# Kernel tuning notes

Hardware: AMD Instinct MI355X
Metric: run time of the kernel (lower is better)

Reference implementation:

```python
import jax, jax.numpy as jnp
import numpy as np

N, E, C = 50000, 800000, 100000
D_IN, HID = 128, 128
MLP_IN, MLP_HID = 2 * HID + 1, HID // 2
BN_EPS = 1e-5
NEG_SLOPE = 0.01


def setup_inputs() -> dict:
    key = jax.random.key(0)
    ks = jax.random.split(key, 24)
    inp = {
        "x": jax.random.normal(ks[0], (N, D_IN), jnp.float32),
        "src": jax.random.randint(ks[1], (E,), 0, N, jnp.int32),
        "dst": jax.random.randint(ks[2], (E,), 0, N, jnp.int32),
        "cand_u": jax.random.randint(ks[3], (C,), 0, N, jnp.int32),
        "cand_v": jax.random.randint(ks[4], (C,), 0, N, jnp.int32),
        "cand_feat": jax.random.normal(ks[5], (C, 1), jnp.float32),
    }
    s = 1.0 / np.sqrt(D_IN)
    # SAGEConv layer 0 and 1 (in=out=128 since statedim == pnhid)
    for li, k0 in [(0, 6), (1, 12)]:
        inp[f"w_self{li}"] = jax.random.uniform(ks[k0], (D_IN, HID), jnp.float32, -s, s)
        inp[f"w_neigh{li}"] = jax.random.uniform(ks[k0 + 1], (D_IN, HID), jnp.float32, -s, s)
        inp[f"b{li}"] = jnp.zeros((HID,), jnp.float32)
        inp[f"gamma{li}"] = jnp.ones((HID,), jnp.float32)
        inp[f"beta{li}"] = jnp.zeros((HID,), jnp.float32)
        inp[f"rm{li}"] = jax.random.normal(ks[k0 + 2], (HID,), jnp.float32) * 0.1
        inp[f"rv{li}"] = jax.random.uniform(ks[k0 + 3], (HID,), jnp.float32, 0.5, 1.5)
    # confidence MLP: 257 -> 64 -> 64 -> 1
    sizes = [MLP_IN, MLP_HID, MLP_HID, 1]
    for i in range(3):
        si = 1.0 / np.sqrt(sizes[i])
        inp[f"mw{i}"] = jax.random.uniform(ks[18 + 2 * i], (sizes[i], sizes[i + 1]), jnp.float32, -si, si)
        inp[f"mb{i}"] = jax.random.uniform(ks[19 + 2 * i], (sizes[i + 1],), jnp.float32, -si, si)
    return inp


def _sage_bn_block(x, src, dst, w_self, w_neigh, b, gamma, beta, rm, rv):
    # mean aggregation over incoming edges (gather -> scatter-add -> divide)
    msgs = x[src]  # [E, D]
    agg = jax.ops.segment_sum(msgs, dst, num_segments=N)  # [N, D]
    deg = jax.ops.segment_sum(jnp.ones((src.shape[0],), x.dtype), dst, num_segments=N)
    agg = agg / jnp.maximum(deg, 1.0)[:, None]
    h = x @ w_self + agg @ w_neigh + b
    # BatchNorm1d (eval mode, running stats) then leaky_relu; dropout is identity in eval
    h = gamma * (h - rm) * jax.lax.rsqrt(rv + BN_EPS) + beta
    return jax.nn.leaky_relu(h, NEG_SLOPE)


def reference(x, src, dst, cand_u, cand_v, cand_feat,
              w_self0, w_neigh0, b0, gamma0, beta0, rm0, rv0,
              w_self1, w_neigh1, b1, gamma1, beta1, rm1, rv1,
              mw0, mb0, mw1, mb1, mw2, mb2):
    h = _sage_bn_block(x, src, dst, w_self0, w_neigh0, b0, gamma0, beta0, rm0, rv0)
    h = _sage_bn_block(h, src, dst, w_self1, w_neigh1, b1, gamma1, beta1, rm1, rv1)
    h = jnp.nan_to_num(h, nan=1e-14)
    # candidate embeddings: [C, 2*HID + 1]
    ce = jnp.concatenate([h[cand_u], h[cand_v], cand_feat], axis=-1)
    z = jax.nn.leaky_relu(ce @ mw0 + mb0, NEG_SLOPE)
    z = jax.nn.leaky_relu(z @ mw1 + mb1, NEG_SLOPE)
    y = z @ mw2 + mb2  # [C, 1]
    return y, jax.nn.softmax(y, axis=0)
```

## Files before the change

### kernel.cpp

```cpp
#include <hip/hip_runtime.h>
#include <math.h>

#define N_NODES 50000
#define N_EDGES 800000
#define N_CAND  100000
#define D       128
#define BN_EPS  1e-5f
#define SLOPE   0.01f

#define NB2     196
#define TILE    4096
#define NTILE   196
#define BCAP    4736

typedef __attribute__((ext_vector_type(8))) short bf16x8;
typedef __attribute__((ext_vector_type(4))) float f32x4;

__device__ __forceinline__ float lrelu(float x){ return x >= 0.f ? x : SLOPE * x; }

__device__ __forceinline__ unsigned short f2bf_rn(float f){
  unsigned int u = __float_as_uint(f);
  unsigned int r = u + 0x7FFFu + ((u >> 16) & 1u);
  return (unsigned short)(r >> 16);
}
__device__ __forceinline__ float bf2f(unsigned short h){
  return __uint_as_float(((unsigned int)h) << 16);
}
__device__ __forceinline__ float4 bf4f(ushort4 u){
  return make_float4(__uint_as_float((unsigned)u.x << 16),
                     __uint_as_float((unsigned)u.y << 16),
                     __uint_as_float((unsigned)u.z << 16),
                     __uint_as_float((unsigned)u.w << 16));
}

__device__ __forceinline__ unsigned pk_bf16(float a, float b){
  unsigned r;
  asm("v_cvt_pk_bf16_f32 %0, %1, %2" : "=v"(r) : "v"(a), "v"(b));
  return r;
}
__device__ __forceinline__ void split2(float a, float b, unsigned &h, unsigned &l){
  h = pk_bf16(a, b);
  float ra = a - __uint_as_float(h << 16);
  float rb = b - __uint_as_float(h & 0xffff0000u);
  l = pk_bf16(ra, rb);
}
__device__ __forceinline__ void split8(const float4 &v0, const float4 &v1, uint4 &h, uint4 &l){
  split2(v0.x, v0.y, h.x, l.x);
  split2(v0.z, v0.w, h.y, l.y);
  split2(v1.x, v1.y, h.z, l.z);
  split2(v1.z, v1.w, h.w, l.w);
}

__global__ __launch_bounds__(256) void k_bin(const int* __restrict__ src, const int* __restrict__ dst,
                                             int* __restrict__ gcnt, unsigned* __restrict__ ebin, int E){
  __shared__ unsigned stage[TILE];
  __shared__ int hist[256], lscan[256], lex[256], lcur[256], gbase[256];
  __shared__ int stot;
  int t = threadIdx.x;
  int e0 = blockIdx.x * TILE;

  hist[t] = 0;
  __syncthreads();

  unsigned pk[16]; int bk[16]; bool ok[16];
  #pragma unroll
  for (int j = 0; j < 16; ++j){
    int i = e0 + j * 256 + t;
    ok[j] = (i < E);
    if (ok[j]){
      int d = dst[i];
      pk[j] = ((unsigned)d << 16) | (unsigned)src[i];
      bk[j] = d >> 8;
      atomicAdd(&hist[bk[j]], 1);
    }
  }
  __syncthreads();

  lscan[t] = hist[t];
  __syncthreads();
  for (int off = 1; off < 256; off <<= 1){
    int v = (t >= off) ? lscan[t - off] : 0;
    __syncthreads();
    lscan[t] += v;
    __syncthreads();
  }
  int ex = lscan[t] - hist[t];
  lex[t]  = ex;
  lcur[t] = ex;
  if (t < NB2) gbase[t] = hist[t] ? atomicAdd(&gcnt[t], hist[t]) : 0;
  if (t == 255) stot = lscan[255];
  __syncthreads();

  #pragma unroll
  for (int j = 0; j < 16; ++j){
    if (ok[j]){
      int p = atomicAdd(&lcur[bk[j]], 1);
      stage[p] = pk[j];
    }
  }
  __syncthreads();

  int tot = stot;
  for (int i = t; i < tot; i += 256){
    unsigned e = stage[i];
    int b = (int)(e >> 24);
    ebin[(size_t)b * BCAP + gbase[b] + (i - lex[b])] = e;
  }
}

__global__ __launch_bounds__(256) void k_bscan2(const int* __restrict__ gcnt, int* __restrict__ bbase,
                                                int* __restrict__ rowptr){
  __shared__ int sd[256];
  int t = threadIdx.x;
  int v = (t < NB2) ? gcnt[t] : 0;
  sd[t] = v; __syncthreads();
  for (int off = 1; off < 256; off <<= 1){
    int a = (t >= off) ? sd[t - off] : 0;
    __syncthreads();
    sd[t] += a; __syncthreads();
  }
  if (t < NB2) bbase[t] = sd[t] - v;
  if (t == NB2 - 1) rowptr[N_NODES] = sd[t];
}

__global__ __launch_bounds__(256) void k_bfin(const int* __restrict__ gcnt, const int* __restrict__ bbase,
                                              const unsigned* __restrict__ ebin,
                                              unsigned short* __restrict__ eid16,
                                              int* __restrict__ rowptr, int n){
  __shared__ int hist[256], lb[256], lcur[256];
  int t = threadIdx.x, b = blockIdx.x;
  int cb   = gcnt[b];
  int base = bbase[b];
  const unsigned* eb = &ebin[(size_t)b * BCAP];
  hist[t] = 0;
  __syncthreads();
  for (int idx = t; idx < cb; idx += 256) atomicAdd(&hist[(eb[idx] >> 16) & 255], 1);
  __syncthreads();
  lb[t] = hist[t];
  __syncthreads();
  for (int off = 1; off < 256; off <<= 1){
    int v = (t >= off) ? lb[t - off] : 0;
    __syncthreads();
    lb[t] += v; __syncthreads();
  }
  int ex = lb[t] - hist[t];
  lcur[t] = ex;
  int node = (b << 8) + t;
  if (node < n) rowptr[node] = base + ex;
  __syncthreads();
  for (int idx = t; idx < cb; idx += 256){
    unsigned e = eb[idx];
    int p = atomicAdd(&lcur[(e >> 16) & 255], 1);
    eid16[base + p] = (unsigned short)(e & 0xffffu);
  }
}

__global__ __launch_bounds__(256) void k_cvt_w(const float* __restrict__ ws, const float* __restrict__ wn,
                                               unsigned short* __restrict__ bth, unsigned short* __restrict__ btl){
  int col = blockIdx.x;
  int k   = threadIdx.x;
  float v = (k < 128) ? ws[k * D + col] : wn[(k - 128) * D + col];
  unsigned short hi = f2bf_rn(v);
  unsigned short lo = f2bf_rn(v - bf2f(hi));
  bth[col * 256 + k] = hi;
  btl[col * 256 + k] = lo;
}

__global__ __launch_bounds__(256) void k_cvt_mlp(const float* __restrict__ w, int K, int Kpad,
                                                 unsigned short* __restrict__ th, unsigned short* __restrict__ tl){
  int col = blockIdx.x;
  for (int k = threadIdx.x; k < Kpad; k += 256){
    float v = (k < K) ? w[k * 64 + col] : 0.f;
    unsigned short hi = f2bf_rn(v);
    th[col * Kpad + k] = hi;
    tl[col * Kpad + k] = f2bf_rn(v - bf2f(hi));
  }
}

__global__ __launch_bounds__(256) void k_cvt_x(const float* __restrict__ X, unsigned short* __restrict__ XB, int nel4){
  int i = blockIdx.x * 256 + threadIdx.x;
  if (i < nel4){
    float4 v = *reinterpret_cast<const float4*>(&X[(size_t)i * 4]);
    ushort4 u;
    u.x = f2bf_rn(v.x); u.y = f2bf_rn(v.y); u.z = f2bf_rn(v.z); u.w = f2bf_rn(v.w);
    *reinterpret_cast<ushort4*>(&XB[(size_t)i * 4]) = u;
  }
}

__global__ __launch_bounds__(256) void k_agg_bf(const unsigned short* __restrict__ XB,
                                                const int* __restrict__ rowptr, const unsigned short* __restrict__ eid,
                                                float* __restrict__ AG, int n){
  int g = blockIdx.x * 8 + (threadIdx.x >> 5);
  int l = threadIdx.x & 31;
  if (g >= n) return;
  int e0 = rowptr[g], e1 = rowptr[g + 1];
  float4 a0 = make_float4(0.f,0.f,0.f,0.f);
  float4 a1 = make_float4(0.f,0.f,0.f,0.f);
  int e = e0;
  for (; e + 2 <= e1; e += 2){
    int s0 = eid[e], s1 = eid[e + 1];
    ushort4 u0 = *reinterpret_cast<const ushort4*>(&XB[(size_t)s0 * D + l * 4]);
    ushort4 u1 = *reinterpret_cast<const ushort4*>(&XB[(size_t)s1 * D + l * 4]);
    float4 f0 = bf4f(u0), f1 = bf4f(u1);
    a0.x += f0.x; a0.y += f0.y; a0.z += f0.z; a0.w += f0.w;
    a1.x += f1.x; a1.y += f1.y; a1.z += f1.z; a1.w += f1.w;
  }
  if (e < e1){
    int s0 = eid[e];
    ushort4 u0 = *reinterpret_cast<const ushort4*>(&XB[(size_t)s0 * D + l * 4]);
    float4 f0 = bf4f(u0);
    a0.x += f0.x; a0.y += f0.y; a0.z += f0.z; a0.w += f0.w;
  }
  float sc = 1.f / fmaxf((float)(e1 - e0), 1.f);
  float4 o;
  o.x = (a0.x + a1.x) * sc; o.y = (a0.y + a1.y) * sc;
  o.z = (a0.z + a1.z) * sc; o.w = (a0.w + a1.w) * sc;
  *reinterpret_cast<float4*>(&AG[(size_t)g * D + l * 4]) = o;
}

__global__ __launch_bounds__(256) void k_sage_mfma(const float* __restrict__ XS, const float* __restrict__ AG,
    const unsigned short* __restrict__ BTH, const unsigned short* __restrict__ BTL,
    const float* __restrict__ Bb, const float* __restrict__ GM, const float* __restrict__ BT,
    const float* __restrict__ RM, const float* __restrict__ RV,
    float* __restrict__ H, unsigned short* __restrict__ HB, int n, int donan)
{
  __shared__ unsigned short Ah[64 * 40];
  __shared__ unsigned short Al[64 * 40];
  __shared__ unsigned short Bh[128 * 40];
  __shared__ unsigned short Bl[128 * 40];

  int t  = threadIdx.x;
  int l  = t & 63;
  int wv = t >> 6;
  int lm = l & 15;
  int lk = l >> 4;
  int node0 = blockIdx.x * 64;

  f32x4 acc[8];
  #pragma unroll
  for (int f = 0; f < 8; ++f) acc[f] = (f32x4){0.f, 0.f, 0.f, 0.f};

  for (int step = 0; step < 8; ++step){
    int k0 = step * 32;
    const float* srcA = (step < 4) ? XS : AG;
    int koff = (step < 4) ? k0 : (k0 - 128);

    __syncthreads();
    #pragma unroll
    for (int i = 0; i < 2; ++i){
      int c   = t + i * 256;
      int row = c >> 3, c4 = c & 7;
      int node = min(node0 + row, n - 1);
      float4 v = *reinterpret_cast<const float4*>(&srcA[(size_t)node * D + koff + c4 * 4]);
      const float* vp = (const float*)&v;
      unsigned short hh[4], ll[4];
      #pragma unroll
      for (int j = 0; j < 4; ++j){
        unsigned short hi = f2bf_rn(vp[j]);
        hh[j] = hi;
        ll[j] = f2bf_rn(vp[j] - bf2f(hi));
      }
      uint2 wh, wl;
      wh.x = (unsigned)hh[0] | ((unsigned)hh[1] << 16);
      wh.y = (unsigned)hh[2] | ((unsigned)hh[3] << 16);
      wl.x = (unsigned)ll[0] | ((unsigned)ll[1] << 16);
      wl.y = (unsigned)ll[2] | ((unsigned)ll[3] << 16);
      *reinterpret_cast<uint2*>(&Ah[row * 40 + c4 * 4]) = wh;
      *reinterpret_cast<uint2*>(&Al[row * 40 + c4 * 4]) = wl;
    }
    #pragma unroll
    for (int i = 0; i < 2; ++i){
      int c   = t + i * 256;
      int col = c >> 2, q = c & 3;
      *reinterpret_cast<uint4*>(&Bh[col * 40 + q * 8]) =
          *reinterpret_cast<const uint4*>(&BTH[col * 256 + k0 + q * 8]);
      *reinterpret_cast<uint4*>(&Bl[col * 40 + q * 8]) =
          *reinterpret_cast<const uint4*>(&BTL[col * 256 + k0 + q * 8]);
    }
    __syncthreads();

    bf16x8 afh = *reinterpret_cast<const bf16x8*>(&Ah[(wv * 16 + lm) * 40 + lk * 8]);
    bf16x8 afl = *reinterpret_cast<const bf16x8*>(&Al[(wv * 16 + lm) * 40 + lk * 8]);
    #pragma unroll
    for (int f = 0; f < 8; ++f){
      bf16x8 bfh = *reinterpret_cast<const bf16x8*>(&Bh[(f * 16 + lm) * 40 + lk * 8]);
      bf16x8 bfl = *reinterpret_cast<const bf16x8*>(&Bl[(f * 16 + lm) * 40 + lk * 8]);
      acc[f] = __builtin_amdgcn_mfma_f32_16x16x32_bf16(afh, bfh, acc[f], 0, 0, 0);
      acc[f] = __builtin_amdgcn_mfma_f32_16x16x32_bf16(afl, bfh, acc[f], 0, 0, 0);
      acc[f] = __builtin_amdgcn_mfma_f32_16x16x32_bf16(afh, bfl, acc[f], 0, 0, 0);
    }
  }

  #pragma unroll
  for (int f = 0; f < 8; ++f){
    int col = f * 16 + lm;
    float s  = GM[col] * rsqrtf(RV[col] + BN_EPS);
    float cj = (Bb[col] - RM[col]) * s + BT[col];
    #pragma unroll
    for (int r = 0; r < 4; ++r){
      int node = node0 + wv * 16 + lk * 4 + r;
      if (node < n){
        float v = lrelu(acc[f][r] * s + cj);
        if (donan && (v != v)) v = 1e-14f;
        H[(size_t)node * D + col] = v;
        if (HB) HB[(size_t)node * D + col] = f2bf_rn(v);
      }
    }
  }
}

__global__ __launch_bounds__(256) void k_mlp_mfma(const float* __restrict__ H,
    const int* __restrict__ cu, const int* __restrict__ cv, const float* __restrict__ cf,
    const unsigned short* __restrict__ W0H, const unsigned short* __restrict__ W0L,
    const float* __restrict__ mw0, const float* __restrict__ mb0,
    const unsigned short* __restrict__ W1H, const unsigned short* __restrict__ W1L,
    const float* __restrict__ mb1, const float* __restrict__ mw2, const float* __restrict__ mb2,
    float* __restrict__ y, int C)
{
  __shared__ unsigned short zh[4][32 * 72];
  __shared__ unsigned short zl[4][32 * 72];

  int t = threadIdx.x;
  int wv = t >> 6, l = t & 63, lm = l & 15, lk = l >> 4;
  int candbase = blockIdx.x * 128 + wv * 32;

  int c0 = min(candbase + lm,      C - 1);
  int c1 = min(candbase + 16 + lm, C - 1);
  int nu0 = cu[c0], nv0 = cv[c0];
  int nu1 = cu[c1], nv1 = cv[c1];

  f32x4 acc[2][4];
  #pragma unroll
  for (int m = 0; m < 2; ++m)
    #pragma unroll
    for (int f = 0; f < 4; ++f) acc[m][f] = (f32x4){0.f, 0.f, 0.f, 0.f};

  #pragma unroll
  for (int s = 0; s < 8; ++s){
    int n0 = (s < 4) ? nu0 : nv0;
    int n1 = (s < 4) ? nu1 : nv1;
    int koff = (s & 3) * 32 + lk * 8;
    const float4* p0 = reinterpret_cast<const float4*>(&H[(size_t)n0 * D + koff]);
    const float4* p1 = reinterpret_cast<const float4*>(&H[(size_t)n1 * D + koff]);
    float4 a00 = p0[0], a01 = p0[1];
    float4 a10 = p1[0], a11 = p1[1];
    uint4 h0, l0, h1, l1;
    split8(a00, a01, h0, l0);
    split8(a10, a11, h1, l1);
    bf16x8 afh0 = *reinterpret_cast<bf16x8*>(&h0);
    bf16x8 afl0 = *reinterpret_cast<bf16x8*>(&l0);
    bf16x8 afh1 = *reinterpret_cast<bf16x8*>(&h1);
    bf16x8 afl1 = *reinterpret_cast<bf16x8*>(&l1);

    int k0 = s * 32 + lk * 8;
    #pragma unroll
    for (int f = 0; f < 4; ++f){
      int col = f * 16 + lm;
      bf16x8 bh = *reinterpret_cast<const bf16x8*>(&W0H[(size_t)col * 264 + k0]);
      bf16x8 bl = *reinterpret_cast<const bf16x8*>(&W0L[(size_t)col * 264 + k0]);
      acc[0][f] = __builtin_amdgcn_mfma_f32_16x16x32_bf16(afh0, bh, acc[0][f], 0, 0, 0);
      acc[0][f] = __builtin_amdgcn_mfma_f32_16x16x32_bf16(afl0, bh, acc[0][f], 0, 0, 0);
      acc[0][f] = __builtin_amdgcn_mfma_f32_16x16x32_bf16(afh0, bl, acc[0][f], 0, 0, 0);
      acc[1][f] = __builtin_amdgcn_mfma_f32_16x16x32_bf16(afh1, bh, acc[1][f], 0, 0, 0);
      acc[1][f] = __builtin_amdgcn_mfma_f32_16x16x32_bf16(afl1, bh, acc[1][f], 0, 0, 0);
      acc[1][f] = __builtin_amdgcn_mfma_f32_16x16x32_bf16(afh1, bl, acc[1][f], 0, 0, 0);
    }
  }

  float cfv[2][4];
  #pragma unroll
  for (int m = 0; m < 2; ++m)
    #pragma unroll
    for (int r = 0; r < 4; ++r)
      cfv[m][r] = cf[min(candbase + m * 16 + lk * 4 + r, C - 1)];

  #pragma unroll
  for (int f = 0; f < 4; ++f){
    int col = f * 16 + lm;
    float b0v = mb0[col];
    float wfv = mw0[256 * 64 + col];
    #pragma unroll
    for (int m = 0; m < 2; ++m){
      #pragma unroll
      for (int r = 0; r < 4; ++r){
        int cl = m * 16 + lk * 4 + r;
        float z = lrelu(acc[m][f][r] + b0v + cfv[m][r] * wfv);
        unsigned short h16 = f2bf_rn(z);
        zh[wv][cl * 72 + col] = h16;
        zl[wv][cl * 72 + col] = f2bf_rn(z - bf2f(h16));
      }
    }
  }

  f32x4 a2[2][4];
  #pragma unroll
  for (int m = 0; m < 2; ++m)
    #pragma unroll
    for (int f = 0; f < 4; ++f) a2[m][f] = (f32x4){0.f, 0.f, 0.f, 0.f};

  #pragma unroll
  for (int s2 = 0; s2 < 2; ++s2){
    int kk = s2 * 32 + lk * 8;
    bf16x8 azh0 = *reinterpret_cast<const bf16x8*>(&zh[wv][(0 * 16 + lm) * 72 + kk]);
    bf16x8 azl0 = *reinterpret_cast<const bf16x8*>(&zl[wv][(0 * 16 + lm) * 72 + kk]);
    bf16x8 azh1 = *reinterpret_cast<const bf16x8*>(&zh[wv][(1 * 16 + lm) * 72 + kk]);
    bf16x8 azl1 = *reinterpret_cast<const bf16x8*>(&zl[wv][(1 * 16 + lm) * 72 + kk]);
    #pragma unroll
    for (int f = 0; f < 4; ++f){
      int col = f * 16 + lm;
      bf16x8 bh = *reinterpret_cast<const bf16x8*>(&W1H[(size_t)col * 64 + kk]);
      bf16x8 bl = *reinterpret_cast<const bf16x8*>(&W1L[(size_t)col * 64 + kk]);
      a2[0][f] = __builtin_amdgcn_mfma_f32_16x16x32_bf16(azh0, bh, a2[0][f], 0, 0, 0);
      a2[0][f] = __builtin_amdgcn_mfma_f32_16x16x32_bf16(azl0, bh, a2[0][f], 0, 0, 0);
      a2[0][f] = __builtin_amdgcn_mfma_f32_16x16x32_bf16(azh0, bl, a2[0][f], 0, 0, 0);
      a2[1][f] = __builtin_amdgcn_mfma_f32_16x16x32_bf16(azh1, bh, a2[1][f], 0, 0, 0);
      a2[1][f] = __builtin_amdgcn_mfma_f32_16x16x32_bf16(azl1, bh, a2[1][f], 0, 0, 0);
      a2[1][f] = __builtin_amdgcn_mfma_f32_16x16x32_bf16(azh1, bl, a2[1][f], 0, 0, 0);
    }
  }

  float p00 = 0.f, p01 = 0.f, p02 = 0.f, p03 = 0.f;
  float p10 = 0.f, p11 = 0.f, p12 = 0.f, p13 = 0.f;
  #pragma unroll
  for (int f = 0; f < 4; ++f){
    int col = f * 16 + lm;
    float b1v = mb1[col];
    float w2v = mw2[col];
    p00 = fmaf(lrelu(a2[0][f][0] + b1v), w2v, p00);
    p01 = fmaf(lrelu(a2[0][f][1] + b1v), w2v, p01);
    p02 = fmaf(lrelu(a2[0][f][2] + b1v), w2v, p02);
    p03 = fmaf(lrelu(a2[0][f][3] + b1v), w2v, p03);
    p10 = fmaf(lrelu(a2[1][f][0] + b1v), w2v, p10);
    p11 = fmaf(lrelu(a2[1][f][1] + b1v), w2v, p11);
    p12 = fmaf(lrelu(a2[1][f][2] + b1v), w2v, p12);
    p13 = fmaf(lrelu(a2[1][f][3] + b1v), w2v, p13);
  }
  #pragma unroll
  for (int off = 1; off < 16; off <<= 1){
    p00 += __shfl_xor(p00, off); p01 += __shfl_xor(p01, off);
    p02 += __shfl_xor(p02, off); p03 += __shfl_xor(p03, off);
    p10 += __shfl_xor(p10, off); p11 += __shfl_xor(p11, off);
    p12 += __shfl_xor(p12, off); p13 += __shfl_xor(p13, off);
  }
  if (lm == 0){
    float b2 = mb2[0];
    int base0 = candbase + lk * 4;
    int base1 = candbase + 16 + lk * 4;
    if (base0 + 0 < C) y[base0 + 0] = p00 + b2;
    if (base0 + 1 < C) y[base0 + 1] = p01 + b2;
    if (base0 + 2 < C) y[base0 + 2] = p02 + b2;
    if (base0 + 3 < C) y[base0 + 3] = p03 + b2;
    if (base1 + 0 < C) y[base1 + 0] = p10 + b2;
    if (base1 + 1 < C) y[base1 + 1] = p11 + b2;
    if (base1 + 2 < C) y[base1 + 2] = p12 + b2;
    if (base1 + 3 < C) y[base1 + 3] = p13 + b2;
  }
}

__global__ __launch_bounds__(256) void k_red1(const float* __restrict__ y,
                                              float* __restrict__ bmax, float* __restrict__ bsum, int C){
  __shared__ float sm[4];
  __shared__ float ss[4];
  int t = threadIdx.x;
  float m = -3.4e38f;
  for (int i = blockIdx.x * 256 + t; i < C; i += gridDim.x * 256) m = fmaxf(m, y[i]);
  for (int o = 32; o; o >>= 1) m = fmaxf(m, __shfl_xor(m, o));
  if ((t & 63) == 0) sm[t >> 6] = m;
  __syncthreads();
  float bm = fmaxf(fmaxf(sm[0], sm[1]), fmaxf(sm[2], sm[3]));
  float s = 0.f;
  for (int i = blockIdx.x * 256 + t; i < C; i += gridDim.x * 256) s += expf(y[i] - bm);
  for (int o = 32; o; o >>= 1) s += __shfl_xor(s, o);
  if ((t & 63) == 0) ss[t >> 6] = s;
  __syncthreads();
  if (t == 0){ bmax[blockIdx.x] = bm; bsum[blockIdx.x] = ss[0] + ss[1] + ss[2] + ss[3]; }
}

__global__ __launch_bounds__(256) void k_red2(const float* __restrict__ bmax, const float* __restrict__ bsum,
                                              float* __restrict__ g, int nb){
  __shared__ float sm[4];
  __shared__ float ss[4];
  int t = threadIdx.x;
  float m0 = (t < nb) ? bmax[t] : -3.4e38f;
  float m = m0;
  for (int o = 32; o; o >>= 1) m = fmaxf(m, __shfl_xor(m, o));
  if ((t & 63) == 0) sm[t >> 6] = m;
  __syncthreads();
  float gm = fmaxf(fmaxf(sm[0], sm[1]), fmaxf(sm[2], sm[3]));
  float s = (t < nb) ? bsum[t] * expf(m0 - gm) : 0.f;
  for (int o = 32; o; o >>= 1) s += __shfl_xor(s, o);
  if ((t & 63) == 0) ss[t >> 6] = s;
  __syncthreads();
  if (t == 0){ g[0] = gm; g[1] = 1.f / (ss[0] + ss[1] + ss[2] + ss[3]); }
}

__global__ __launch_bounds__(256) void k_red3(const float* __restrict__ y, const float* __restrict__ g,
                                              float* __restrict__ out, int C){
  int i = blockIdx.x * 256 + threadIdx.x;
  if (i < C) out[i] = expf(y[i] - g[0]) * g[1];
}

extern "C" void kernel_launch(void* const* d_in, const int* in_sizes, int n_in,
                              void* d_out, int out_size, void* d_ws, size_t ws_size,
                              hipStream_t stream)
{
  const float* x   = (const float*)d_in[0];
  const int*   src = (const int*)  d_in[1];
  const int*   dst = (const int*)  d_in[2];
  const int*   cu  = (const int*)  d_in[3];
  const int*   cv  = (const int*)  d_in[4];
  const float* cf  = (const float*)d_in[5];
  const float* ws0 = (const float*)d_in[6];
  const float* wn0 = (const float*)d_in[7];
  const float* b0  = (const float*)d_in[8];
  const float* g0  = (const float*)d_in[9];
  const float* be0 = (const float*)d_in[10];
  const float* rm0 = (const float*)d_in[11];
  const float* rv0 = (const float*)d_in[12];
  const float* ws1 = (const float*)d_in[13];
  const float* wn1 = (const float*)d_in[14];
  const float* b1  = (const float*)d_in[15];
  const float* g1  = (const float*)d_in[16];
  const float* be1 = (const float*)d_in[17];
  const float* rm1 = (const float*)d_in[18];
  const float* rv1 = (const float*)d_in[19];
  const float* mw0 = (const float*)d_in[20];
  const float* mb0 = (const float*)d_in[21];
  const float* mw1 = (const float*)d_in[22];
  const float* mb1 = (const float*)d_in[23];
  const float* mw2 = (const float*)d_in[24];
  const float* mb2 = (const float*)d_in[25];

  float* out = (float*)d_out;

  char* w = (char*)d_ws;
  float* aggn  = (float*)w; w += (size_t)N_NODES * D * 4;
  float* h0    = (float*)w; w += (size_t)N_NODES * D * 4;
  float* h1    = (float*)w; w += (size_t)N_NODES * D * 4;
  int* cnt     = (int*)w;   w += (size_t)N_NODES * 4;
  int* rowptr  = (int*)w;   w += (size_t)(N_NODES + 1) * 4;
  int* cur     = (int*)w;   w += (size_t)N_NODES * 4;
  int* eid     = (int*)w;   w += (size_t)N_EDGES * 4;
  int* gcnt    = (int*)w;   w += (size_t)(NB2 + 8) * 4;
  int* bbase   = (int*)w;   w += (size_t)(NB2 + 1) * 4;
  float* bmax  = (float*)w; w += 256 * 4;
  float* bsumF = (float*)w; w += 256 * 4;
  float* gred  = (float*)w; w += 2 * 4;
  unsigned short* w0th = (unsigned short*)w; w += (size_t)64 * 264 * 2;
  unsigned short* w0tl = (unsigned short*)w; w += (size_t)64 * 264 * 2;
  unsigned short* w1th = (unsigned short*)w; w += (size_t)64 * 64 * 2;
  unsigned short* w1tl = (unsigned short*)w; w += (size_t)64 * 64 * 2;

  unsigned short* eid16 = (unsigned short*)eid;

  unsigned* ebin = (unsigned*)h0;

  unsigned short* xb  = (unsigned short*)h1;
  unsigned short* hb0 = xb + (size_t)N_NODES * D;

  unsigned short* bth0 = (unsigned short*)cnt;
  unsigned short* btl0 = bth0 + 128 * 256;
  unsigned short* bth1 = (unsigned short*)cur;
  unsigned short* btl1 = bth1 + 128 * 256;

  hipMemsetAsync(gcnt, 0, (size_t)NB2 * 4, stream);
  k_bin   <<<NTILE, 256, 0, stream>>>(src, dst, gcnt, ebin, N_EDGES);
  k_bscan2<<<1, 256, 0, stream>>>(gcnt, bbase, rowptr);
  k_bfin  <<<NB2, 256, 0, stream>>>(gcnt, bbase, ebin, eid16, rowptr, N_NODES);

  k_cvt_w<<<128, 256, 0, stream>>>(ws0, wn0, bth0, btl0);
  k_cvt_w<<<128, 256, 0, stream>>>(ws1, wn1, bth1, btl1);
  k_cvt_mlp<<<64, 256, 0, stream>>>(mw0, 257, 264, w0th, w0tl);
  k_cvt_mlp<<<64, 256, 0, stream>>>(mw1, 64, 64, w1th, w1tl);
  k_cvt_x<<<(N_NODES * D / 4 + 255) / 256, 256, 0, stream>>>(x, xb, N_NODES * D / 4);

  int GB = (N_NODES + 63) / 64;
  k_agg_bf<<<(N_NODES + 7) / 8, 256, 0, stream>>>(xb, rowptr, eid16, aggn, N_NODES);
  k_sage_mfma<<<GB, 256, 0, stream>>>(x,  aggn, bth0, btl0, b0, g0, be0, rm0, rv0, h0, hb0, N_NODES, 0);
  k_agg_bf<<<(N_NODES + 7) / 8, 256, 0, stream>>>(hb0, rowptr, eid16, aggn, N_NODES);
  k_sage_mfma<<<GB, 256, 0, stream>>>(h0, aggn, bth1, btl1, b1, g1, be1, rm1, rv1, h1, (unsigned short*)0, N_NODES, 1);

  k_mlp_mfma<<<(N_CAND + 127) / 128, 256, 0, stream>>>(h1, cu, cv, cf,
      w0th, w0tl, mw0, mb0, w1th, w1tl, mb1, mw2, mb2, out, N_CAND);

  k_red1<<<256, 256, 0, stream>>>(out, bmax, bsumF, N_CAND);
  k_red2<<<1, 256, 0, stream>>>(bmax, bsumF, gred, 256);
  k_red3<<<(N_CAND + 255) / 256, 256, 0, stream>>>(out, gred, out + N_CAND, N_CAND);
}
```

Baseline: 235.4 us.

## Emit split bf16 hi/lo from layer-2 SAGE, prefetch MLP gathers, unroll aggregation

The second SAGE kernel now writes the final embedding directly as bf16 high and low halves instead of fp32. The MLP then loads these pre-split operands, so it no longer converts and splits the gathered rows itself. The MLP loop also prefetches the next step's gathered rows before issuing the current MFMAs, and the neighbour aggregation is unrolled to four edges per iteration for more loads in flight. Both versions write and gather the same number of bytes per node row. The cost is one extra rounding in the epilogue and more registers held live in the MLP.

```diff
diff --git a/kernel.cpp b/kernel.cpp
--- a/kernel.cpp
+++ b/kernel.cpp
@@ -31,24 +31,6 @@
                      __uint_as_float((unsigned)u.y << 16),
                      __uint_as_float((unsigned)u.z << 16),
                      __uint_as_float((unsigned)u.w << 16));
-}
-
-__device__ __forceinline__ unsigned pk_bf16(float a, float b){
-  unsigned r;
-  asm("v_cvt_pk_bf16_f32 %0, %1, %2" : "=v"(r) : "v"(a), "v"(b));
-  return r;
-}
-__device__ __forceinline__ void split2(float a, float b, unsigned &h, unsigned &l){
-  h = pk_bf16(a, b);
-  float ra = a - __uint_as_float(h << 16);
-  float rb = b - __uint_as_float(h & 0xffff0000u);
-  l = pk_bf16(ra, rb);
-}
-__device__ __forceinline__ void split8(const float4 &v0, const float4 &v1, uint4 &h, uint4 &l){
-  split2(v0.x, v0.y, h.x, l.x);
-  split2(v0.z, v0.w, h.y, l.y);
-  split2(v1.x, v1.y, h.z, l.z);
-  split2(v1.z, v1.w, h.w, l.w);
 }
 
 __global__ __launch_bounds__(256) void k_bin(const int* __restrict__ src, const int* __restrict__ dst,
@@ -196,16 +178,22 @@
   int e0 = rowptr[g], e1 = rowptr[g + 1];
   float4 a0 = make_float4(0.f,0.f,0.f,0.f);
   float4 a1 = make_float4(0.f,0.f,0.f,0.f);
+  float4 a2 = make_float4(0.f,0.f,0.f,0.f);
+  float4 a3 = make_float4(0.f,0.f,0.f,0.f);
   int e = e0;
-  for (; e + 2 <= e1; e += 2){
-    int s0 = eid[e], s1 = eid[e + 1];
+  for (; e + 4 <= e1; e += 4){
+    int s0 = eid[e], s1 = eid[e + 1], s2 = eid[e + 2], s3 = eid[e + 3];
     ushort4 u0 = *reinterpret_cast<const ushort4*>(&XB[(size_t)s0 * D + l * 4]);
     ushort4 u1 = *reinterpret_cast<const ushort4*>(&XB[(size_t)s1 * D + l * 4]);
-    float4 f0 = bf4f(u0), f1 = bf4f(u1);
+    ushort4 u2 = *reinterpret_cast<const ushort4*>(&XB[(size_t)s2 * D + l * 4]);
+    ushort4 u3 = *reinterpret_cast<const ushort4*>(&XB[(size_t)s3 * D + l * 4]);
+    float4 f0 = bf4f(u0), f1 = bf4f(u1), f2 = bf4f(u2), f3 = bf4f(u3);
     a0.x += f0.x; a0.y += f0.y; a0.z += f0.z; a0.w += f0.w;
     a1.x += f1.x; a1.y += f1.y; a1.z += f1.z; a1.w += f1.w;
-  }
-  if (e < e1){
+    a2.x += f2.x; a2.y += f2.y; a2.z += f2.z; a2.w += f2.w;
+    a3.x += f3.x; a3.y += f3.y; a3.z += f3.z; a3.w += f3.w;
+  }
+  for (; e < e1; ++e){
     int s0 = eid[e];
     ushort4 u0 = *reinterpret_cast<const ushort4*>(&XB[(size_t)s0 * D + l * 4]);
     float4 f0 = bf4f(u0);
@@ -213,8 +201,10 @@
   }
   float sc = 1.f / fmaxf((float)(e1 - e0), 1.f);
   float4 o;
-  o.x = (a0.x + a1.x) * sc; o.y = (a0.y + a1.y) * sc;
-  o.z = (a0.z + a1.z) * sc; o.w = (a0.w + a1.w) * sc;
+  o.x = (a0.x + a1.x + a2.x + a3.x) * sc;
+  o.y = (a0.y + a1.y + a2.y + a3.y) * sc;
+  o.z = (a0.z + a1.z + a2.z + a3.z) * sc;
+  o.w = (a0.w + a1.w + a2.w + a3.w) * sc;
   *reinterpret_cast<float4*>(&AG[(size_t)g * D + l * 4]) = o;
 }
 
@@ -222,7 +212,8 @@
     const unsigned short* __restrict__ BTH, const unsigned short* __restrict__ BTL,
     const float* __restrict__ Bb, const float* __restrict__ GM, const float* __restrict__ BT,
     const float* __restrict__ RM, const float* __restrict__ RV,
-    float* __restrict__ H, unsigned short* __restrict__ HB, int n, int donan)
+    float* __restrict__ H, unsigned short* __restrict__ HBH, unsigned short* __restrict__ HBL,
+    int n, int donan)
 {
   __shared__ unsigned short Ah[64 * 40];
   __shared__ unsigned short Al[64 * 40];
@@ -302,14 +293,17 @@
       if (node < n){
         float v = lrelu(acc[f][r] * s + cj);
         if (donan && (v != v)) v = 1e-14f;
-        H[(size_t)node * D + col] = v;
-        if (HB) HB[(size_t)node * D + col] = f2bf_rn(v);
+        if (H)  H[(size_t)node * D + col] = v;
+        unsigned short h16 = f2bf_rn(v);
+        if (HBH) HBH[(size_t)node * D + col] = h16;
+        if (HBL) HBL[(size_t)node * D + col] = f2bf_rn(v - bf2f(h16));
       }
     }
   }
 }
 
-__global__ __launch_bounds__(256) void k_mlp_mfma(const float* __restrict__ H,
+__global__ __launch_bounds__(256) void k_mlp_mfma(
+    const unsigned short* __restrict__ HH, const unsigned short* __restrict__ HL,
     const int* __restrict__ cu, const int* __restrict__ cv, const float* __restrict__ cf,
     const unsigned short* __restrict__ W0H, const unsigned short* __restrict__ W0L,
     const float* __restrict__ mw0, const float* __restrict__ mb0,
@@ -335,36 +329,38 @@
     #pragma unroll
     for (int f = 0; f < 4; ++f) acc[m][f] = (f32x4){0.f, 0.f, 0.f, 0.f};
 
+  int kbase = lk * 8;
+  bf16x8 ah0 = *reinterpret_cast<const bf16x8*>(&HH[(size_t)nu0 * D + kbase]);
+  bf16x8 al0 = *reinterpret_cast<const bf16x8*>(&HL[(size_t)nu0 * D + kbase]);
+  bf16x8 ah1 = *reinterpret_cast<const bf16x8*>(&HH[(size_t)nu1 * D + kbase]);
+  bf16x8 al1 = *reinterpret_cast<const bf16x8*>(&HL[(size_t)nu1 * D + kbase]);
+
   #pragma unroll
   for (int s = 0; s < 8; ++s){
-    int n0 = (s < 4) ? nu0 : nv0;
-    int n1 = (s < 4) ? nu1 : nv1;
-    int koff = (s & 3) * 32 + lk * 8;
-    const float4* p0 = reinterpret_cast<const float4*>(&H[(size_t)n0 * D + koff]);
-    const float4* p1 = reinterpret_cast<const float4*>(&H[(size_t)n1 * D + koff]);
-    float4 a00 = p0[0], a01 = p0[1];
-    float4 a10 = p1[0], a11 = p1[1];
-    uint4 h0, l0, h1, l1;
-    split8(a00, a01, h0, l0);
-    split8(a10, a11, h1, l1);
-    bf16x8 afh0 = *reinterpret_cast<bf16x8*>(&h0);
-    bf16x8 afl0 = *reinterpret_cast<bf16x8*>(&l0);
-    bf16x8 afh1 = *reinterpret_cast<bf16x8*>(&h1);
-    bf16x8 afl1 = *reinterpret_cast<bf16x8*>(&l1);
-
-    int k0 = s * 32 + lk * 8;
+    bf16x8 nh0, nl0, nh1, nl1;
+    if (s < 7){
+      int n0 = (s + 1 < 4) ? nu0 : nv0;
+      int n1 = (s + 1 < 4) ? nu1 : nv1;
+      int koff = ((s + 1) & 3) * 32 + kbase;
+      nh0 = *reinterpret_cast<const bf16x8*>(&HH[(size_t)n0 * D + koff]);
+      nl0 = *reinterpret_cast<const bf16x8*>(&HL[(size_t)n0 * D + koff]);
+      nh1 = *reinterpret_cast<const bf16x8*>(&HH[(size_t)n1 * D + koff]);
+      nl1 = *reinterpret_cast<const bf16x8*>(&HL[(size_t)n1 * D + koff]);
+    }
+    int k0 = s * 32 + kbase;
     #pragma unroll
     for (int f = 0; f < 4; ++f){
       int col = f * 16 + lm;
       bf16x8 bh = *reinterpret_cast<const bf16x8*>(&W0H[(size_t)col * 264 + k0]);
       bf16x8 bl = *reinterpret_cast<const bf16x8*>(&W0L[(size_t)col * 264 + k0]);
-      acc[0][f] = __builtin_amdgcn_mfma_f32_16x16x32_bf16(afh0, bh, acc[0][f], 0, 0, 0);
-      acc[0][f] = __builtin_amdgcn_mfma_f32_16x16x32_bf16(afl0, bh, acc[0][f], 0, 0, 0);
-      acc[0][f] = __builtin_amdgcn_mfma_f32_16x16x32_bf16(afh0, bl, acc[0][f], 0, 0, 0);
-      acc[1][f] = __builtin_amdgcn_mfma_f32_16x16x32_bf16(afh1, bh, acc[1][f], 0, 0, 0);
-      acc[1][f] = __builtin_amdgcn_mfma_f32_16x16x32_bf16(afl1, bh, acc[1][f], 0, 0, 0);
-      acc[1][f] = __builtin_amdgcn_mfma_f32_16x16x32_bf16(afh1, bl, acc[1][f], 0, 0, 0);
-    }
+      acc[0][f] = __builtin_amdgcn_mfma_f32_16x16x32_bf16(ah0, bh, acc[0][f], 0, 0, 0);
+      acc[0][f] = __builtin_amdgcn_mfma_f32_16x16x32_bf16(al0, bh, acc[0][f], 0, 0, 0);
+      acc[0][f] = __builtin_amdgcn_mfma_f32_16x16x32_bf16(ah0, bl, acc[0][f], 0, 0, 0);
+      acc[1][f] = __builtin_amdgcn_mfma_f32_16x16x32_bf16(ah1, bh, acc[1][f], 0, 0, 0);
+      acc[1][f] = __builtin_amdgcn_mfma_f32_16x16x32_bf16(al1, bh, acc[1][f], 0, 0, 0);
+      acc[1][f] = __builtin_amdgcn_mfma_f32_16x16x32_bf16(ah1, bl, acc[1][f], 0, 0, 0);
+    }
+    if (s < 7){ ah0 = nh0; al0 = nl0; ah1 = nh1; al1 = nl1; }
   }
 
   float cfv[2][4];
@@ -400,7 +396,7 @@
 
   #pragma unroll
   for (int s2 = 0; s2 < 2; ++s2){
-    int kk = s2 * 32 + lk * 8;
+    int kk = s2 * 32 + kbase;
     bf16x8 azh0 = *reinterpret_cast<const bf16x8*>(&zh[wv][(0 * 16 + lm) * 72 + kk]);
     bf16x8 azl0 = *reinterpret_cast<const bf16x8*>(&zl[wv][(0 * 16 + lm) * 72 + kk]);
     bf16x8 azh1 = *reinterpret_cast<const bf16x8*>(&zh[wv][(1 * 16 + lm) * 72 + kk]);
@@ -555,8 +551,10 @@
 
   unsigned* ebin = (unsigned*)h0;
 
-  unsigned short* xb  = (unsigned short*)h1;
-  unsigned short* hb0 = xb + (size_t)N_NODES * D;
+  unsigned short* xb   = (unsigned short*)h1;
+  unsigned short* hb0  = xb + (size_t)N_NODES * D;
+  unsigned short* hb1h = (unsigned short*)h1;
+  unsigned short* hb1l = hb1h + (size_t)N_NODES * D;
 
   unsigned short* bth0 = (unsigned short*)cnt;
   unsigned short* btl0 = bth0 + 128 * 256;
@@ -576,11 +574,13 @@
 
   int GB = (N_NODES + 63) / 64;
   k_agg_bf<<<(N_NODES + 7) / 8, 256, 0, stream>>>(xb, rowptr, eid16, aggn, N_NODES);
-  k_sage_mfma<<<GB, 256, 0, stream>>>(x,  aggn, bth0, btl0, b0, g0, be0, rm0, rv0, h0, hb0, N_NODES, 0);
+  k_sage_mfma<<<GB, 256, 0, stream>>>(x,  aggn, bth0, btl0, b0, g0, be0, rm0, rv0,
+                                      h0, hb0, (unsigned short*)0, N_NODES, 0);
   k_agg_bf<<<(N_NODES + 7) / 8, 256, 0, stream>>>(hb0, rowptr, eid16, aggn, N_NODES);
-  k_sage_mfma<<<GB, 256, 0, stream>>>(h0, aggn, bth1, btl1, b1, g1, be1, rm1, rv1, h1, (unsigned short*)0, N_NODES, 1);
-
-  k_mlp_mfma<<<(N_CAND + 127) / 128, 256, 0, stream>>>(h1, cu, cv, cf,
+  k_sage_mfma<<<GB, 256, 0, stream>>>(h0, aggn, bth1, btl1, b1, g1, be1, rm1, rv1,
+                                      (float*)0, hb1h, hb1l, N_NODES, 1);
+
+  k_mlp_mfma<<<(N_CAND + 127) / 128, 256, 0, stream>>>(hb1h, hb1l, cu, cv, cf,
       w0th, w0tl, mw0, mb0, w1th, w1tl, mb1, mw2, mb2, out, N_CAND);
 
   k_red1<<<256, 256, 0, stream>>>(out, bmax, bsumF, N_CAND);
```

Measured after the change: 230.2 us. -2.2%, faster.
